# Kernel tuning notes

Hardware: AMD Instinct MI355X
Metric: run time of the kernel (lower is better)

Reference implementation:

```python
import jax, jax.numpy as jnp
import numpy as np

HEAD_DIM = 32
KERNEL = 9
DILATION = 3


def setup_inputs() -> dict:
    key = jax.random.key(0)
    k1, k2, k3 = jax.random.split(key, 3)
    B, d, L = 4, 512, 4096
    q = jax.random.normal(k1, (B, d, 1, L), dtype=jnp.float32)
    k = jax.random.normal(k2, (B, d, 1, L), dtype=jnp.float32)
    v = jax.random.normal(k3, (B, d, 1, L), dtype=jnp.float32)
    return {"q": q, "k": k, "v": v}


def reference(q, k, v):
    # q,k,v: [B, d, 1, L]; output: [B, 1, L, d]
    B, d, _, N = q.shape
    hd = HEAD_DIM
    h = d // hd
    K = KERNEL
    dil = DILATION
    pad = dil * (K - 1) // 2
    scale = hd ** -0.5

    # Window gather indices replicating nn.Unfold with zero padding.
    idx = jnp.arange(N)[:, None] + jnp.arange(K)[None, :] * dil - pad  # [N, K]
    valid = ((idx >= 0) & (idx < N)).astype(q.dtype)                   # [N, K]
    idxc = jnp.clip(idx, 0, N - 1)

    qr = q.reshape(B, h, hd, N)
    kr = k.reshape(B, h, hd, N)
    vr = v.reshape(B, h, hd, N)

    # Unfolded windows: [B, h, hd, N, K], zero outside bounds (like Unfold padding)
    kw = kr[:, :, :, idxc] * valid
    vw = vr[:, :, :, idxc] * valid

    attn = jnp.einsum('bhdn,bhdnk->bhnk', qr, kw) * scale
    attn = jax.nn.softmax(attn, axis=-1)
    out = jnp.einsum('bhnk,bhdnk->bhnd', attn, vw)  # [B, h, N, hd]
    # torch: transpose(1,2).reshape(B,1,N,d) -> heads concatenated per token
    return out.transpose(0, 2, 1, 3).reshape(B, 1, N, d)
```

## Files before the change

### kernel.cpp

```cpp
#include <hip/hip_runtime.h>
#include <math.h>

#define NPOS 4096
#define DCH  512
#define HD   32
#define NH   16
#define KW   9
#define DIL  3
#define PAD  12
#define TILE   128
#define NTILES (NPOS / TILE)
#define SPANT  (TILE + 2*PAD)
#define ROWF4  (SPANT / 4)
#define SLDS   156
#define CSPL   8
#define CPT    (HD / CSPL)
#define TPT    4
#define WSPAN  28

__global__ __launch_bounds__(256) void dilate_attn_kernel(
    const float* __restrict__ q,
    const float* __restrict__ k,
    const float* __restrict__ v,
    float* __restrict__ out)
{
    __shared__ float ks[HD * SLDS];
    __shared__ float vs[HD * SLDS];

    const int bh   = blockIdx.x >> 5;
    const int tile = blockIdx.x & (NTILES - 1);
    const int n0t  = tile * TILE;
    const int ws   = n0t - PAD;

    const size_t cb = (size_t)bh * HD * NPOS;
    const float* kg = k + cb;
    const float* vg = v + cb;
    const float* qg = q + cb;

    const bool easy = (ws >= 0) && (ws + SPANT <= NPOS);
    for (int p = threadIdx.x; p < HD * ROWF4; p += 256) {
        int row = p / ROWF4;
        int c4  = p - row * ROWF4;
        int g0  = ws + c4 * 4;
        const float* kr = kg + (size_t)row * NPOS;
        const float* vr = vg + (size_t)row * NPOS;
        float4 kk, vv;
        if (easy || (g0 >= 0 && g0 + 4 <= NPOS)) {
            kk = *(const float4*)(kr + g0);
            vv = *(const float4*)(vr + g0);
        } else {
            int i0 = min(max(g0 + 0, 0), NPOS - 1);
            int i1 = min(max(g0 + 1, 0), NPOS - 1);
            int i2 = min(max(g0 + 2, 0), NPOS - 1);
            int i3 = min(max(g0 + 3, 0), NPOS - 1);
            kk = make_float4(kr[i0], kr[i1], kr[i2], kr[i3]);
            vv = make_float4(vr[i0], vr[i1], vr[i2], vr[i3]);
        }
        *(float4*)&ks[row * SLDS + c4 * 4] = kk;
        *(float4*)&vs[row * SLDS + c4 * 4] = vv;
    }

    const int cs = threadIdx.x & (CSPL - 1);
    const int lg = threadIdx.x >> 3;
    const int n0 = n0t + lg * TPT;

    float4 qv[CPT];
#pragma unroll
    for (int i = 0; i < CPT; ++i) {
        int ch = cs * CPT + i;
        qv[i] = *(const float4*)(qg + (size_t)ch * NPOS + n0);
    }

    __syncthreads();

    float s[TPT][KW];
#pragma unroll
    for (int t = 0; t < TPT; ++t)
#pragma unroll
        for (int j = 0; j < KW; ++j) s[t][j] = 0.0f;

#pragma unroll
    for (int i = 0; i < CPT; ++i) {
        int row = cs * CPT + i;
        const float4* wp = (const float4*)&ks[row * SLDS + lg * TPT];
        float w[WSPAN];
#pragma unroll
        for (int u = 0; u < WSPAN / 4; ++u) {
            float4 x = wp[u];
            w[4*u] = x.x; w[4*u+1] = x.y; w[4*u+2] = x.z; w[4*u+3] = x.w;
        }
        float qt[TPT] = {qv[i].x, qv[i].y, qv[i].z, qv[i].w};
#pragma unroll
        for (int t = 0; t < TPT; ++t)
#pragma unroll
            for (int j = 0; j < KW; ++j)
                s[t][j] = fmaf(qt[t], w[t + 3*j], s[t][j]);
    }

#pragma unroll
    for (int t = 0; t < TPT; ++t)
#pragma unroll
        for (int j = 0; j < KW; ++j) {
            float x = s[t][j];
            x += __shfl_xor(x, 1);
            x += __shfl_xor(x, 2);
            x += __shfl_xor(x, 4);
            s[t][j] = x;
        }

    const float scale = 0.17677669529663687f;
#pragma unroll
    for (int t = 0; t < TPT; ++t) {
        float m = -INFINITY;
#pragma unroll
        for (int j = 0; j < KW; ++j) {
            float valid = ((unsigned)(n0 + t + 3*j - PAD) < NPOS) ? 1.0f : 0.0f;
            float x = s[t][j] * scale * valid;
            s[t][j] = x;
            m = fmaxf(m, x);
        }
        float sum = 0.0f;
#pragma unroll
        for (int j = 0; j < KW; ++j) {
            float e = __expf(s[t][j] - m);
            s[t][j] = e;
            sum += e;
        }
        float inv = 1.0f / sum;
#pragma unroll
        for (int j = 0; j < KW; ++j) {
            float valid = ((unsigned)(n0 + t + 3*j - PAD) < NPOS) ? 1.0f : 0.0f;
            s[t][j] *= inv * valid;
        }
    }

    float o[TPT][CPT];
#pragma unroll
    for (int t = 0; t < TPT; ++t)
#pragma unroll
        for (int i = 0; i < CPT; ++i) o[t][i] = 0.0f;

#pragma unroll
    for (int i = 0; i < CPT; ++i) {
        int row = cs * CPT + i;
        const float4* wp = (const float4*)&vs[row * SLDS + lg * TPT];
        float w[WSPAN];
#pragma unroll
        for (int u = 0; u < WSPAN / 4; ++u) {
            float4 x = wp[u];
            w[4*u] = x.x; w[4*u+1] = x.y; w[4*u+2] = x.z; w[4*u+3] = x.w;
        }
#pragma unroll
        for (int t = 0; t < TPT; ++t)
#pragma unroll
            for (int j = 0; j < KW; ++j)
                o[t][i] = fmaf(s[t][j], w[t + 3*j], o[t][i]);
    }

    const int b  = bh >> 4;
    const int hh = bh & (NH - 1);
#pragma unroll
    for (int t = 0; t < TPT; ++t) {
        float* op = out + ((size_t)(b * NPOS + n0 + t)) * DCH + hh * HD + cs * CPT;
        *(float4*)op = make_float4(o[t][0], o[t][1], o[t][2], o[t][3]);
    }
}

extern "C" void kernel_launch(void* const* d_in, const int* in_sizes, int n_in,
                              void* d_out, int out_size, void* d_ws, size_t ws_size,
                              hipStream_t stream) {
    const float* q = (const float*)d_in[0];
    const float* k = (const float*)d_in[1];
    const float* v = (const float*)d_in[2];
    float* out = (float*)d_out;

    const int grid = 4 * NH * NTILES;
    hipLaunchKernelGGL(dilate_attn_kernel, dim3(grid), dim3(256), 0, stream,
                       q, k, v, out);
}
```

Baseline: 145.8 us.

## Load K/V tiles via direct global-to-LDS loads and use DPP reductions

For interior tiles, K and V windows are loaded with global_load_lds, which writes straight into shared memory and skips the round trip through registers. The cross-lane sum over 8 channel groups switches from shuffles to DPP row operations. Interior tiles also get a softmax path without the validity masking. This is meant to cut load latency and register pressure during staging, and to lower reduction overhead. The risk is that the DPP control codes and the LDS layout the direct load produces must match what the old per-thread float4 stores wrote.

Result: faster. 142.9 us (-2.0%).

```diff
diff --git a/kernel.cpp b/kernel.cpp
--- a/kernel.cpp
+++ b/kernel.cpp
@@ -13,10 +13,30 @@
 #define SPANT  (TILE + 2*PAD)
 #define ROWF4  (SPANT / 4)
 #define SLDS   156
+#define ROWC   (SLDS / 4)
+#define NCHK   (HD * ROWC)
 #define CSPL   8
 #define CPT    (HD / CSPL)
 #define TPT    4
 #define WSPAN  28
+
+__device__ __forceinline__ void gload16(const float* g, float* l) {
+    __builtin_amdgcn_global_load_lds(
+        (const __attribute__((address_space(1))) void*)g,
+        (__attribute__((address_space(3))) void*)l,
+        16, 0, 0);
+}
+
+__device__ __forceinline__ float dpp_sum8(float x) {
+    int t;
+    t = __builtin_amdgcn_update_dpp(0, __float_as_int(x), 0xB1, 0xF, 0xF, true);
+    x += __int_as_float(t);
+    t = __builtin_amdgcn_update_dpp(0, __float_as_int(x), 0x4E, 0xF, 0xF, true);
+    x += __int_as_float(t);
+    t = __builtin_amdgcn_update_dpp(0, __float_as_int(x), 0x141, 0xF, 0xF, true);
+    x += __int_as_float(t);
+    return x;
+}
 
 __global__ __launch_bounds__(256) void dilate_attn_kernel(
     const float* __restrict__ q,
@@ -24,8 +44,9 @@
     const float* __restrict__ v,
     float* __restrict__ out)
 {
-    __shared__ float ks[HD * SLDS];
-    __shared__ float vs[HD * SLDS];
+    __shared__ float kv[2 * HD * SLDS];
+    float* const ks = kv;
+    float* const vs = kv + HD * SLDS;
 
     const int bh   = blockIdx.x >> 5;
     const int tile = blockIdx.x & (NTILES - 1);
@@ -38,26 +59,50 @@
     const float* qg = q + cb;
 
     const bool easy = (ws >= 0) && (ws + SPANT <= NPOS);
-    for (int p = threadIdx.x; p < HD * ROWF4; p += 256) {
-        int row = p / ROWF4;
-        int c4  = p - row * ROWF4;
-        int g0  = ws + c4 * 4;
-        const float* kr = kg + (size_t)row * NPOS;
-        const float* vr = vg + (size_t)row * NPOS;
-        float4 kk, vv;
-        if (easy || (g0 >= 0 && g0 + 4 <= NPOS)) {
-            kk = *(const float4*)(kr + g0);
-            vv = *(const float4*)(vr + g0);
-        } else {
-            int i0 = min(max(g0 + 0, 0), NPOS - 1);
-            int i1 = min(max(g0 + 1, 0), NPOS - 1);
-            int i2 = min(max(g0 + 2, 0), NPOS - 1);
-            int i3 = min(max(g0 + 3, 0), NPOS - 1);
-            kk = make_float4(kr[i0], kr[i1], kr[i2], kr[i3]);
-            vv = make_float4(vr[i0], vr[i1], vr[i2], vr[i3]);
-        }
-        *(float4*)&ks[row * SLDS + c4 * 4] = kk;
-        *(float4*)&vs[row * SLDS + c4 * 4] = vv;
+
+    if (easy) {
+#pragma unroll
+        for (int it = 0; it < 5; ++it) {
+            int c = it * 256 + (int)threadIdx.x;
+            if (c < NCHK) {
+                int row = c / ROWC;
+                int c4  = c - row * ROWC;
+                gload16(kg + (size_t)row * NPOS + (ws + c4 * 4),
+                        &kv[(size_t)c * 4]);
+            }
+        }
+#pragma unroll
+        for (int it = 0; it < 5; ++it) {
+            int c = it * 256 + (int)threadIdx.x;
+            if (c < NCHK) {
+                int row = c / ROWC;
+                int c4  = c - row * ROWC;
+                gload16(vg + (size_t)row * NPOS + (ws + c4 * 4),
+                        &kv[(size_t)(NCHK + c) * 4]);
+            }
+        }
+    } else {
+        for (int p = threadIdx.x; p < HD * ROWF4; p += 256) {
+            int row = p / ROWF4;
+            int c4  = p - row * ROWF4;
+            int g0  = ws + c4 * 4;
+            const float* kr = kg + (size_t)row * NPOS;
+            const float* vr = vg + (size_t)row * NPOS;
+            float4 kk, vv;
+            if (g0 >= 0 && g0 + 4 <= NPOS) {
+                kk = *(const float4*)(kr + g0);
+                vv = *(const float4*)(vr + g0);
+            } else {
+                int i0 = min(max(g0 + 0, 0), NPOS - 1);
+                int i1 = min(max(g0 + 1, 0), NPOS - 1);
+                int i2 = min(max(g0 + 2, 0), NPOS - 1);
+                int i3 = min(max(g0 + 3, 0), NPOS - 1);
+                kk = make_float4(kr[i0], kr[i1], kr[i2], kr[i3]);
+                vv = make_float4(vr[i0], vr[i1], vr[i2], vr[i3]);
+            }
+            *(float4*)&ks[row * SLDS + c4 * 4] = kk;
+            *(float4*)&vs[row * SLDS + c4 * 4] = vv;
+        }
     }
 
     const int cs = threadIdx.x & (CSPL - 1);
@@ -100,37 +145,54 @@
 #pragma unroll
     for (int t = 0; t < TPT; ++t)
 #pragma unroll
-        for (int j = 0; j < KW; ++j) {
-            float x = s[t][j];
-            x += __shfl_xor(x, 1);
-            x += __shfl_xor(x, 2);
-            x += __shfl_xor(x, 4);
-            s[t][j] = x;
-        }
+        for (int j = 0; j < KW; ++j)
+            s[t][j] = dpp_sum8(s[t][j]);
 
     const float scale = 0.17677669529663687f;
-#pragma unroll
-    for (int t = 0; t < TPT; ++t) {
-        float m = -INFINITY;
-#pragma unroll
-        for (int j = 0; j < KW; ++j) {
-            float valid = ((unsigned)(n0 + t + 3*j - PAD) < NPOS) ? 1.0f : 0.0f;
-            float x = s[t][j] * scale * valid;
-            s[t][j] = x;
-            m = fmaxf(m, x);
-        }
-        float sum = 0.0f;
-#pragma unroll
-        for (int j = 0; j < KW; ++j) {
-            float e = __expf(s[t][j] - m);
-            s[t][j] = e;
-            sum += e;
-        }
-        float inv = 1.0f / sum;
-#pragma unroll
-        for (int j = 0; j < KW; ++j) {
-            float valid = ((unsigned)(n0 + t + 3*j - PAD) < NPOS) ? 1.0f : 0.0f;
-            s[t][j] *= inv * valid;
+    if (easy) {
+#pragma unroll
+        for (int t = 0; t < TPT; ++t) {
+            float m = -INFINITY;
+#pragma unroll
+            for (int j = 0; j < KW; ++j) {
+                float x = s[t][j] * scale;
+                s[t][j] = x;
+                m = fmaxf(m, x);
+            }
+            float sum = 0.0f;
+#pragma unroll
+            for (int j = 0; j < KW; ++j) {
+                float e = __expf(s[t][j] - m);
+                s[t][j] = e;
+                sum += e;
+            }
+            float inv = 1.0f / sum;
+#pragma unroll
+            for (int j = 0; j < KW; ++j) s[t][j] *= inv;
+        }
+    } else {
+#pragma unroll
+        for (int t = 0; t < TPT; ++t) {
+            float vm[KW];
+            float m = -INFINITY;
+#pragma unroll
+            for (int j = 0; j < KW; ++j) {
+                vm[j] = ((unsigned)(n0 + t + 3*j - PAD) < NPOS) ? 1.0f : 0.0f;
+                float x = s[t][j] * scale * vm[j];
+                s[t][j] = x;
+                m = fmaxf(m, x);
+            }
+            float sum = 0.0f;
+#pragma unroll
+            for (int j = 0; j < KW; ++j) {
+                float e = __expf(s[t][j] - m);
+                s[t][j] = e;
+                sum += e;
+            }
+            float inv = 1.0f / sum;
+#pragma unroll
+            for (int j = 0; j < KW; ++j)
+                s[t][j] *= inv * vm[j];
         }
     }
 
```
